# Performance work log

Hardware: AMD Instinct MI355X
Metric: run time of the kernel (lower is better)

Reference implementation:

```python
import jax, jax.numpy as jnp
import numpy as np

BS = 4096
D = 256
TAU = 0.5
EPS = 1e-08          # eps added to negative-sum denominator (module arg)
COS_EPS = 1e-08      # nn.CosineSimilarity norm clamp


def setup_inputs() -> dict:
    key = jax.random.key(0)
    k1, k2 = jax.random.split(key)
    zi = jax.random.normal(k1, (BS, D), dtype=jnp.float32)
    zj = jax.random.normal(k2, (BS, D), dtype=jnp.float32)
    return {"zi": zi, "zj": zj}


def reference(zi, zj):
    bs = zi.shape[0]
    n = 2 * bs
    z = jnp.concatenate([zi, zj], axis=0)                       # [2bs, D]
    # cosine similarity = normalized dot products (norms clamped like torch)
    norm = jnp.linalg.norm(z, axis=-1, keepdims=True)
    zn = z / jnp.maximum(norm, COS_EPS)
    sim = jnp.matmul(zn, zn.T) / TAU                            # [2bs, 2bs]
    e = jnp.exp(sim)
    # positive pairs: row i pairs with column (i+bs) mod 2bs
    rows = jnp.arange(n)
    pair = jnp.concatenate([jnp.arange(bs) + bs, jnp.arange(bs)])
    sim_pos = e[rows, pair]                                     # [2bs]
    # negatives: all entries in a row except the diagonal
    sim_neg_sum = e.sum(axis=-1) - jnp.diagonal(e)              # [2bs]
    loss = jnp.mean(-jnp.log(sim_pos / (sim_neg_sum + EPS)))
    return loss
```

## Files before the change

kernel.cpp:

```cpp
#include <hip/hip_runtime.h>
#include <hip/hip_bf16.h>


#define N_ROWS 8192
#define BSZ    4096
#define DIM    256
#define INV_TAU 2.0f
#define EPS_REF 1e-8f
#define COS_EPS 1e-8f
#define NG2     64
#define NTILES  (NG2 * (NG2 + 1) / 2)
#define LSTRIDE 260

typedef __attribute__((ext_vector_type(4))) float f32x4;
typedef __attribute__((ext_vector_type(8))) int   v8i;
typedef union { int4 x[2]; v8i v; } frag32;

__device__ __forceinline__ float red16(float x) {
    x += __int_as_float(__builtin_amdgcn_update_dpp(0, __float_as_int(x), 0x121, 0xf, 0xf, false));
    x += __int_as_float(__builtin_amdgcn_update_dpp(0, __float_as_int(x), 0x122, 0xf, 0xf, false));
    x += __int_as_float(__builtin_amdgcn_update_dpp(0, __float_as_int(x), 0x124, 0xf, 0xf, false));
    x += __int_as_float(__builtin_amdgcn_update_dpp(0, __float_as_int(x), 0x128, 0xf, 0xf, false));
    return x;
}

__global__ __launch_bounds__(256) void knorm(const float* __restrict__ zi,
                                             const float* __restrict__ zj,
                                             unsigned char* __restrict__ znsw,
                                             float* __restrict__ out) {
    __shared__ float lds[16 * LSTRIDE];
    __shared__ float nrm[16];
    const int rg = blockIdx.x;
    const int t  = threadIdx.x;
    const int w  = t >> 6;
    const int l  = t & 63;
    const int row0 = rg * 16;
    if (rg == 0 && t == 0) out[0] = 0.f;

    #pragma unroll
    for (int s = 0; s < 4; ++s) {
        const int row = s * 4 + w;
        const int r   = row0 + row;
        const float* src = (r < BSZ) ? zi + (size_t)r * DIM + l * 4
                                     : zj + (size_t)(r - BSZ) * DIM + l * 4;
        const float4 v = *(const float4*)src;
        *(float4*)&lds[row * LSTRIDE + l * 4] = v;
        float ss = v.x*v.x + v.y*v.y + v.z*v.z + v.w*v.w;
        #pragma unroll
        for (int off = 32; off >= 1; off >>= 1) ss += __shfl_xor(ss, off);
        if (l == 0) nrm[row] = 1.0f / fmaxf(sqrtf(ss), COS_EPS);
    }
    __syncthreads();

    const int pi = t >> 6, fl = t & 63;
    const int h = pi >> 1, p = pi & 1;
    const int r16 = fl & 15, q = fl >> 4;
    const int k0 = h * 128 + q * 32 + p * 16;
    const float inv = nrm[r16];
    float f[16];
    #pragma unroll
    for (int j = 0; j < 16; ++j) f[j] = lds[r16 * LSTRIDE + k0 + j] * inv;
    int wd[4];
    #pragma unroll
    for (int g = 0; g < 4; ++g) {
        int a = 0;
        a = __builtin_amdgcn_cvt_pk_fp8_f32(f[g*4+0], f[g*4+1], a, false);
        a = __builtin_amdgcn_cvt_pk_fp8_f32(f[g*4+2], f[g*4+3], a, true);
        wd[g] = a;
    }
    *(int4*)(znsw + (size_t)rg * 4096 + pi * 1024 + fl * 16) =
        make_int4(wd[0], wd[1], wd[2], wd[3]);
}

__global__ __launch_bounds__(256, 3) void kgemm(const unsigned char* __restrict__ znsw,
                                                float* __restrict__ P,
                                                float* __restrict__ selfdot,
                                                float* __restrict__ pairdot) {
    __shared__ __align__(16) unsigned char pan[32768];
    const int w = threadIdx.x >> 6;
    const int l = threadIdx.x & 63;

    const int t = blockIdx.x;
    int Gi = (int)((129.0f - sqrtf(16641.0f - 8.0f * (float)t)) * 0.5f);
    while ((Gi + 1) * (129 - (Gi + 1)) / 2 <= t) ++Gi;
    while (Gi * (129 - Gi) / 2 > t) --Gi;
    const int Gj = Gi + (t - Gi * (129 - Gi) / 2);

    const char* srcA = (const char*)znsw + (size_t)Gi * 32768;
    #pragma unroll
    for (int sub = 0; sub < 8; ++sub) {
        const int off = sub * 4096 + w * 1024;
        __builtin_amdgcn_global_load_lds(
            (const __attribute__((address_space(1))) void*)(srcA + off + l * 16),
            (__attribute__((address_space(3))) void*)(&pan[off]), 16, 0, 0);
    }

    const int rh = w >> 1, ch = w & 1;
    const char* bbase = (const char*)znsw + (size_t)Gj * 32768 + ch * 16384 + l * 16;

    frag32 B[4];
    #pragma unroll
    for (int nt = 0; nt < 4; ++nt) {
        B[nt].x[0] = *(const int4*)(bbase + nt * 4096);
        B[nt].x[1] = *(const int4*)(bbase + nt * 4096 + 1024);
    }

    f32x4 acc[4][4];
    #pragma unroll
    for (int mt = 0; mt < 4; ++mt)
        #pragma unroll
        for (int nt = 0; nt < 4; ++nt)
            acc[mt][nt] = (f32x4){0.f, 0.f, 0.f, 0.f};

    __syncthreads();

    #pragma unroll
    for (int h = 0; h < 2; ++h) {
        if (h == 1) {
            #pragma unroll
            for (int nt = 0; nt < 4; ++nt) {
                B[nt].x[0] = *(const int4*)(bbase + nt * 4096 + 2048);
                B[nt].x[1] = *(const int4*)(bbase + nt * 4096 + 3072);
            }
        }
        #pragma unroll
        for (int mt = 0; mt < 4; ++mt) {
            frag32 A;
            const char* ap = (const char*)&pan[(rh * 4 + mt) * 4096 + h * 2048] + l * 16;
            A.x[0] = *(const int4*)(ap);
            A.x[1] = *(const int4*)(ap + 1024);
            #pragma unroll
            for (int nt = 0; nt < 4; ++nt)
                acc[mt][nt] = __builtin_amdgcn_mfma_scale_f32_16x16x128_f8f6f4(
                    A.v, B[nt].v, acc[mt][nt],
                    0, 0,
                    0, 0x7f7f7f7f,
                    0, 0x7f7f7f7f);
        }
    }

    const int c = l & 15, q = l >> 4;
    const int rsel = c - 4 * q;
    const bool vld = (rsel >= 0) && (rsel < 4);

    if ((Gi == Gj || Gj == Gi + 32) && rh == ch) {
        float dv[4];
        #pragma unroll
        for (int mt = 0; mt < 4; ++mt) {
            float d = acc[mt][mt][0];
            #pragma unroll
            for (int r = 1; r < 4; ++r)
                if (rsel == r) d = acc[mt][mt][r];
            dv[mt] = d;
        }
        if (vld) {
            float* dst = (Gi == Gj) ? selfdot : pairdot;
            #pragma unroll
            for (int mt = 0; mt < 4; ++mt)
                dst[Gi * 128 + rh * 64 + mt * 16 + c] = dv[mt];
        }
    }

    #pragma unroll
    for (int mt = 0; mt < 4; ++mt)
        #pragma unroll
        for (int nt = 0; nt < 4; ++nt)
            #pragma unroll
            for (int r = 0; r < 4; ++r)
                acc[mt][nt][r] = __expf(acc[mt][nt][r] * INV_TAU);

    float rs[4][4];
    #pragma unroll
    for (int mt = 0; mt < 4; ++mt)
        #pragma unroll
        for (int r = 0; r < 4; ++r)
            rs[mt][r] = red16(acc[mt][0][r] + acc[mt][1][r] + acc[mt][2][r] + acc[mt][3][r]);
    if (c == 0) {
        #pragma unroll
        for (int mt = 0; mt < 4; ++mt) {
            const f32x4 o4 = (f32x4){rs[mt][0], rs[mt][1], rs[mt][2], rs[mt][3]};
            __builtin_nontemporal_store(o4,
                (f32x4*)&P[(size_t)(Gj * 2 + ch) * N_ROWS + Gi * 128 + rh * 64 + mt * 16 + q * 4]);
        }
    }

    if (Gi != Gj) {
        float cs[4];
        #pragma unroll
        for (int nt = 0; nt < 4; ++nt) {
            float s = 0.f;
            #pragma unroll
            for (int mt = 0; mt < 4; ++mt)
                #pragma unroll
                for (int r = 0; r < 4; ++r)
                    s += acc[mt][nt][r];
            s += __shfl_xor(s, 16);
            s += __shfl_xor(s, 32);
            cs[nt] = s;
        }
        if (q == 0) {
            #pragma unroll
            for (int nt = 0; nt < 4; ++nt)
                __builtin_nontemporal_store(cs[nt],
                    &P[(size_t)(Gi * 2 + rh) * N_ROWS + Gj * 128 + ch * 64 + nt * 16 + c]);
        }
    }
}

__global__ __launch_bounds__(256) void kfinal(const float* __restrict__ P,
                                              const float* __restrict__ selfdot,
                                              const float* __restrict__ pairdot,
                                              float* __restrict__ out) {
    const int l = threadIdx.x & 63;
    const int w = threadIdx.x >> 6;
    const int row = blockIdx.x * 64 + l;
    float s = 0.f;
    #pragma unroll
    for (int st = 0; st < 32; ++st)
        s += P[(size_t)(w * 32 + st) * N_ROWS + row];
    __shared__ float wsum[4][64];
    wsum[w][l] = s;
    __syncthreads();
    if (w == 0) {
        const float tot = wsum[0][l] + wsum[1][l] + wsum[2][l] + wsum[3][l];
        const float selfe = __expf(selfdot[row] * INV_TAU);
        const float pd    = pairdot[(row < BSZ) ? row : row - BSZ];
        float loss = logf(tot - selfe + EPS_REF) - pd * INV_TAU;
        #pragma unroll
        for (int off = 32; off >= 1; off >>= 1) loss += __shfl_xor(loss, off);
        if (l == 0) atomicAdd(out, loss * (1.0f / (float)N_ROWS));
    }
}

extern "C" void kernel_launch(void* const* d_in, const int* in_sizes, int n_in,
                              void* d_out, int out_size, void* d_ws, size_t ws_size,
                              hipStream_t stream) {
    const float* zi = (const float*)d_in[0];
    const float* zj = (const float*)d_in[1];
    float* out = (float*)d_out;

    char* ws = (char*)d_ws;
    unsigned char* znsw = (unsigned char*)ws;
    float* P       = (float*)(ws + 2 * 1024 * 1024);
    float* selfdot = (float*)(ws + 6 * 1024 * 1024);
    float* pairdot = (float*)(ws + 6 * 1024 * 1024 + 32 * 1024);

    knorm <<<N_ROWS / 16, 256, 0, stream>>>(zi, zj, znsw, out);
    kgemm <<<NTILES, 256, 0, stream>>>(znsw, P, selfdot, pairdot);
    kfinal<<<N_ROWS / 64, 256, 0, stream>>>(P, selfdot, pairdot, out);
}
```

Measured before the change: 82.96 us.

## Fuse final loss reduction into GEMM via atomics and last-block tail

Partial row sums of exp(sim) are no longer written to a large partial-sum matrix for a separate reduction kernel. Each tile now atomically adds them into a per-row accumulator. The last block to finish, found through an atomic completion counter, computes the log terms and writes the mean loss. This removes the third kernel launch and the partial-matrix traffic. In exchange it adds contention from many float atomics, a serialized single-block tail over 8192 rows, and non-deterministic summation order.

```diff
diff --git a/kernel.cpp b/kernel.cpp
--- a/kernel.cpp
+++ b/kernel.cpp
@@ -27,7 +27,8 @@
 __global__ __launch_bounds__(256) void knorm(const float* __restrict__ zi,
                                              const float* __restrict__ zj,
                                              unsigned char* __restrict__ znsw,
-                                             float* __restrict__ out) {
+                                             float* __restrict__ rowsum,
+                                             unsigned int* __restrict__ done) {
     __shared__ float lds[16 * LSTRIDE];
     __shared__ float nrm[16];
     const int rg = blockIdx.x;
@@ -35,7 +36,9 @@
     const int w  = t >> 6;
     const int l  = t & 63;
     const int row0 = rg * 16;
-    if (rg == 0 && t == 0) out[0] = 0.f;
+
+    if (t < 16) rowsum[rg * 16 + t] = 0.f;
+    if (rg == 0 && t == 16) *done = 0u;
 
     #pragma unroll
     for (int s = 0; s < 4; ++s) {
@@ -73,10 +76,14 @@
 }
 
 __global__ __launch_bounds__(256, 3) void kgemm(const unsigned char* __restrict__ znsw,
-                                                float* __restrict__ P,
+                                                float* __restrict__ rowsum,
                                                 float* __restrict__ selfdot,
-                                                float* __restrict__ pairdot) {
+                                                float* __restrict__ pairdot,
+                                                unsigned int* __restrict__ done,
+                                                float* __restrict__ out) {
     __shared__ __align__(16) unsigned char pan[32768];
+    __shared__ float tailred[4];
+    __shared__ int   islast;
     const int w = threadIdx.x >> 6;
     const int l = threadIdx.x & 63;
 
@@ -157,7 +164,8 @@
             float* dst = (Gi == Gj) ? selfdot : pairdot;
             #pragma unroll
             for (int mt = 0; mt < 4; ++mt)
-                dst[Gi * 128 + rh * 64 + mt * 16 + c] = dv[mt];
+                __hip_atomic_store(&dst[Gi * 128 + rh * 64 + mt * 16 + c], dv[mt],
+                                   __ATOMIC_RELAXED, __HIP_MEMORY_SCOPE_AGENT);
         }
     }
 
@@ -177,11 +185,10 @@
             rs[mt][r] = red16(acc[mt][0][r] + acc[mt][1][r] + acc[mt][2][r] + acc[mt][3][r]);
     if (c == 0) {
         #pragma unroll
-        for (int mt = 0; mt < 4; ++mt) {
-            const f32x4 o4 = (f32x4){rs[mt][0], rs[mt][1], rs[mt][2], rs[mt][3]};
-            __builtin_nontemporal_store(o4,
-                (f32x4*)&P[(size_t)(Gj * 2 + ch) * N_ROWS + Gi * 128 + rh * 64 + mt * 16 + q * 4]);
-        }
+        for (int mt = 0; mt < 4; ++mt)
+            #pragma unroll
+            for (int r = 0; r < 4; ++r)
+                atomicAdd(&rowsum[Gi * 128 + rh * 64 + mt * 16 + q * 4 + r], rs[mt][r]);
     }
 
     if (Gi != Gj) {
@@ -201,35 +208,36 @@
         if (q == 0) {
             #pragma unroll
             for (int nt = 0; nt < 4; ++nt)
-                __builtin_nontemporal_store(cs[nt],
-                    &P[(size_t)(Gi * 2 + rh) * N_ROWS + Gj * 128 + ch * 64 + nt * 16 + c]);
-        }
-    }
-}
-
-__global__ __launch_bounds__(256) void kfinal(const float* __restrict__ P,
-                                              const float* __restrict__ selfdot,
-                                              const float* __restrict__ pairdot,
-                                              float* __restrict__ out) {
-    const int l = threadIdx.x & 63;
-    const int w = threadIdx.x >> 6;
-    const int row = blockIdx.x * 64 + l;
-    float s = 0.f;
-    #pragma unroll
-    for (int st = 0; st < 32; ++st)
-        s += P[(size_t)(w * 32 + st) * N_ROWS + row];
-    __shared__ float wsum[4][64];
-    wsum[w][l] = s;
-    __syncthreads();
-    if (w == 0) {
-        const float tot = wsum[0][l] + wsum[1][l] + wsum[2][l] + wsum[3][l];
-        const float selfe = __expf(selfdot[row] * INV_TAU);
-        const float pd    = pairdot[(row < BSZ) ? row : row - BSZ];
-        float loss = logf(tot - selfe + EPS_REF) - pd * INV_TAU;
-        #pragma unroll
-        for (int off = 32; off >= 1; off >>= 1) loss += __shfl_xor(loss, off);
-        if (l == 0) atomicAdd(out, loss * (1.0f / (float)N_ROWS));
-    }
+                atomicAdd(&rowsum[Gj * 128 + ch * 64 + nt * 16 + c], cs[nt]);
+        }
+    }
+
+    __syncthreads();
+    if (threadIdx.x == 0) {
+        unsigned int old = __hip_atomic_fetch_add(done, 1u, __ATOMIC_ACQ_REL,
+                                                  __HIP_MEMORY_SCOPE_AGENT);
+        islast = (old == NTILES - 1);
+    }
+    __syncthreads();
+    if (!islast) return;
+
+    float part = 0.f;
+    for (int i = 0; i < N_ROWS / 256; ++i) {
+        const int row = i * 256 + threadIdx.x;
+        const float tot = __hip_atomic_load(&rowsum[row], __ATOMIC_RELAXED,
+                                            __HIP_MEMORY_SCOPE_AGENT);
+        const float sd  = __hip_atomic_load(&selfdot[row], __ATOMIC_RELAXED,
+                                            __HIP_MEMORY_SCOPE_AGENT);
+        const float pd  = __hip_atomic_load(&pairdot[(row < BSZ) ? row : row - BSZ],
+                                            __ATOMIC_RELAXED, __HIP_MEMORY_SCOPE_AGENT);
+        part += logf(tot - __expf(sd * INV_TAU) + EPS_REF) - pd * INV_TAU;
+    }
+    #pragma unroll
+    for (int off = 32; off >= 1; off >>= 1) part += __shfl_xor(part, off);
+    if (l == 0) tailred[w] = part;
+    __syncthreads();
+    if (threadIdx.x == 0)
+        out[0] = (tailred[0] + tailred[1] + tailred[2] + tailred[3]) * (1.0f / (float)N_ROWS);
 }
 
 extern "C" void kernel_launch(void* const* d_in, const int* in_sizes, int n_in,
@@ -241,11 +249,11 @@
 
     char* ws = (char*)d_ws;
     unsigned char* znsw = (unsigned char*)ws;
-    float* P       = (float*)(ws + 2 * 1024 * 1024);
-    float* selfdot = (float*)(ws + 6 * 1024 * 1024);
-    float* pairdot = (float*)(ws + 6 * 1024 * 1024 + 32 * 1024);
-
-    knorm <<<N_ROWS / 16, 256, 0, stream>>>(zi, zj, znsw, out);
-    kgemm <<<NTILES, 256, 0, stream>>>(znsw, P, selfdot, pairdot);
-    kfinal<<<N_ROWS / 64, 256, 0, stream>>>(P, selfdot, pairdot, out);
-}
+    float* rowsum  = (float*)(ws + 2 * 1024 * 1024);
+    float* selfdot = (float*)(ws + 2 * 1024 * 1024 + 32 * 1024);
+    float* pairdot = (float*)(ws + 2 * 1024 * 1024 + 64 * 1024);
+    unsigned int* done = (unsigned int*)(ws + 2 * 1024 * 1024 + 80 * 1024);
+
+    knorm <<<N_ROWS / 16, 256, 0, stream>>>(zi, zj, znsw, rowsum, done);
+    kgemm <<<NTILES, 256, 0, stream>>>(znsw, rowsum, selfdot, pairdot, done, out);
+}
```

New measurement: 116.7 us. +40.7%, slower.

## Fuse GEMM and final reduction into persistent kernel with grid-wide atomic barrier

Applied to the files above, without the earlier changes.

Merges the tile GEMM kernel and the final loss reduction into one persistent kernel of 512 blocks that loop over the triangular tiles. A global atomic counter acts as a grid barrier, after which the first 128 blocks run the per-row reduction and loss accumulation. This removes one kernel launch and the launch gap between them. In exchange, the former vector nontemporal stores become scalar relaxed atomic stores, and the spin-wait assumes all 512 blocks are co-resident, which risks deadlock if occupancy is lower.

```diff
diff --git a/kernel.cpp b/kernel.cpp
--- a/kernel.cpp
+++ b/kernel.cpp
@@ -10,6 +10,8 @@
 #define COS_EPS 1e-8f
 #define NG2     64
 #define NTILES  (NG2 * (NG2 + 1) / 2)
+#define GRID2   512
+#define PH3BLK  128
 #define LSTRIDE 260
 
 typedef __attribute__((ext_vector_type(4))) float f32x4;
@@ -27,6 +29,7 @@
 __global__ __launch_bounds__(256) void knorm(const float* __restrict__ zi,
                                              const float* __restrict__ zj,
                                              unsigned char* __restrict__ znsw,
+                                             unsigned int* __restrict__ cnt,
                                              float* __restrict__ out) {
     __shared__ float lds[16 * LSTRIDE];
     __shared__ float nrm[16];
@@ -35,7 +38,8 @@
     const int w  = t >> 6;
     const int l  = t & 63;
     const int row0 = rg * 16;
-    if (rg == 0 && t == 0) out[0] = 0.f;
+    if (rg == 0 && t == 0)  out[0] = 0.f;
+    if (rg == 0 && t == 16) *cnt = 0u;
 
     #pragma unroll
     for (int s = 0; s < 4; ++s) {
@@ -72,159 +76,173 @@
         make_int4(wd[0], wd[1], wd[2], wd[3]);
 }
 
-__global__ __launch_bounds__(256, 3) void kgemm(const unsigned char* __restrict__ znsw,
-                                                float* __restrict__ P,
-                                                float* __restrict__ selfdot,
-                                                float* __restrict__ pairdot) {
+__global__ __launch_bounds__(256, 3) void kfused(const unsigned char* __restrict__ znsw,
+                                                 float* __restrict__ P,
+                                                 float* __restrict__ selfdot,
+                                                 float* __restrict__ pairdot,
+                                                 unsigned int* __restrict__ cnt,
+                                                 float* __restrict__ out) {
     __shared__ __align__(16) unsigned char pan[32768];
+    __shared__ float wsum[4][64];
     const int w = threadIdx.x >> 6;
     const int l = threadIdx.x & 63;
-
-    const int t = blockIdx.x;
-    int Gi = (int)((129.0f - sqrtf(16641.0f - 8.0f * (float)t)) * 0.5f);
-    while ((Gi + 1) * (129 - (Gi + 1)) / 2 <= t) ++Gi;
-    while (Gi * (129 - Gi) / 2 > t) --Gi;
-    const int Gj = Gi + (t - Gi * (129 - Gi) / 2);
-
-    const char* srcA = (const char*)znsw + (size_t)Gi * 32768;
-    #pragma unroll
-    for (int sub = 0; sub < 8; ++sub) {
-        const int off = sub * 4096 + w * 1024;
-        __builtin_amdgcn_global_load_lds(
-            (const __attribute__((address_space(1))) void*)(srcA + off + l * 16),
-            (__attribute__((address_space(3))) void*)(&pan[off]), 16, 0, 0);
-    }
-
     const int rh = w >> 1, ch = w & 1;
-    const char* bbase = (const char*)znsw + (size_t)Gj * 32768 + ch * 16384 + l * 16;
-
-    frag32 B[4];
-    #pragma unroll
-    for (int nt = 0; nt < 4; ++nt) {
-        B[nt].x[0] = *(const int4*)(bbase + nt * 4096);
-        B[nt].x[1] = *(const int4*)(bbase + nt * 4096 + 1024);
-    }
-
-    f32x4 acc[4][4];
-    #pragma unroll
-    for (int mt = 0; mt < 4; ++mt)
-        #pragma unroll
-        for (int nt = 0; nt < 4; ++nt)
-            acc[mt][nt] = (f32x4){0.f, 0.f, 0.f, 0.f};
-
-    __syncthreads();
-
-    #pragma unroll
-    for (int h = 0; h < 2; ++h) {
-        if (h == 1) {
-            #pragma unroll
-            for (int nt = 0; nt < 4; ++nt) {
-                B[nt].x[0] = *(const int4*)(bbase + nt * 4096 + 2048);
-                B[nt].x[1] = *(const int4*)(bbase + nt * 4096 + 3072);
-            }
-        }
-        #pragma unroll
-        for (int mt = 0; mt < 4; ++mt) {
-            frag32 A;
-            const char* ap = (const char*)&pan[(rh * 4 + mt) * 4096 + h * 2048] + l * 16;
-            A.x[0] = *(const int4*)(ap);
-            A.x[1] = *(const int4*)(ap + 1024);
-            #pragma unroll
-            for (int nt = 0; nt < 4; ++nt)
-                acc[mt][nt] = __builtin_amdgcn_mfma_scale_f32_16x16x128_f8f6f4(
-                    A.v, B[nt].v, acc[mt][nt],
-                    0, 0,
-                    0, 0x7f7f7f7f,
-                    0, 0x7f7f7f7f);
-        }
-    }
-
     const int c = l & 15, q = l >> 4;
     const int rsel = c - 4 * q;
     const bool vld = (rsel >= 0) && (rsel < 4);
 
-    if ((Gi == Gj || Gj == Gi + 32) && rh == ch) {
-        float dv[4];
-        #pragma unroll
-        for (int mt = 0; mt < 4; ++mt) {
-            float d = acc[mt][mt][0];
-            #pragma unroll
-            for (int r = 1; r < 4; ++r)
-                if (rsel == r) d = acc[mt][mt][r];
-            dv[mt] = d;
-        }
-        if (vld) {
-            float* dst = (Gi == Gj) ? selfdot : pairdot;
+    for (int t = blockIdx.x; t < NTILES; t += GRID2) {
+        int Gi = (int)((129.0f - sqrtf(16641.0f - 8.0f * (float)t)) * 0.5f);
+        while ((Gi + 1) * (129 - (Gi + 1)) / 2 <= t) ++Gi;
+        while (Gi * (129 - Gi) / 2 > t) --Gi;
+        const int Gj = Gi + (t - Gi * (129 - Gi) / 2);
+
+        __syncthreads();
+
+        const char* srcA = (const char*)znsw + (size_t)Gi * 32768;
+        #pragma unroll
+        for (int sub = 0; sub < 8; ++sub) {
+            const int off = sub * 4096 + w * 1024;
+            __builtin_amdgcn_global_load_lds(
+                (const __attribute__((address_space(1))) void*)(srcA + off + l * 16),
+                (__attribute__((address_space(3))) void*)(&pan[off]), 16, 0, 0);
+        }
+
+        const char* bbase = (const char*)znsw + (size_t)Gj * 32768 + ch * 16384 + l * 16;
+
+        frag32 B[4];
+        #pragma unroll
+        for (int nt = 0; nt < 4; ++nt) {
+            B[nt].x[0] = *(const int4*)(bbase + nt * 4096);
+            B[nt].x[1] = *(const int4*)(bbase + nt * 4096 + 1024);
+        }
+
+        f32x4 acc[4][4];
+        #pragma unroll
+        for (int mt = 0; mt < 4; ++mt)
+            #pragma unroll
+            for (int nt = 0; nt < 4; ++nt)
+                acc[mt][nt] = (f32x4){0.f, 0.f, 0.f, 0.f};
+
+        __syncthreads();
+
+        #pragma unroll
+        for (int h = 0; h < 2; ++h) {
+            if (h == 1) {
+                #pragma unroll
+                for (int nt = 0; nt < 4; ++nt) {
+                    B[nt].x[0] = *(const int4*)(bbase + nt * 4096 + 2048);
+                    B[nt].x[1] = *(const int4*)(bbase + nt * 4096 + 3072);
+                }
+            }
+            #pragma unroll
+            for (int mt = 0; mt < 4; ++mt) {
+                frag32 A;
+                const char* ap = (const char*)&pan[(rh * 4 + mt) * 4096 + h * 2048] + l * 16;
+                A.x[0] = *(const int4*)(ap);
+                A.x[1] = *(const int4*)(ap + 1024);
+                #pragma unroll
+                for (int nt = 0; nt < 4; ++nt)
+                    acc[mt][nt] = __builtin_amdgcn_mfma_scale_f32_16x16x128_f8f6f4(
+                        A.v, B[nt].v, acc[mt][nt],
+                        0, 0,
+                        0, 0x7f7f7f7f,
+                        0, 0x7f7f7f7f);
+            }
+        }
+
+        if ((Gi == Gj || Gj == Gi + 32) && rh == ch) {
+            float dv[4];
+            #pragma unroll
+            for (int mt = 0; mt < 4; ++mt) {
+                float d = acc[mt][mt][0];
+                #pragma unroll
+                for (int r = 1; r < 4; ++r)
+                    if (rsel == r) d = acc[mt][mt][r];
+                dv[mt] = d;
+            }
+            if (vld) {
+                float* dst = (Gi == Gj) ? selfdot : pairdot;
+                #pragma unroll
+                for (int mt = 0; mt < 4; ++mt)
+                    __hip_atomic_store(&dst[Gi * 128 + rh * 64 + mt * 16 + c], dv[mt],
+                                       __ATOMIC_RELAXED, __HIP_MEMORY_SCOPE_AGENT);
+            }
+        }
+
+        #pragma unroll
+        for (int mt = 0; mt < 4; ++mt)
+            #pragma unroll
+            for (int nt = 0; nt < 4; ++nt)
+                #pragma unroll
+                for (int r = 0; r < 4; ++r)
+                    acc[mt][nt][r] = __expf(acc[mt][nt][r] * INV_TAU);
+
+        float rs[4][4];
+        #pragma unroll
+        for (int mt = 0; mt < 4; ++mt)
+            #pragma unroll
+            for (int r = 0; r < 4; ++r)
+                rs[mt][r] = red16(acc[mt][0][r] + acc[mt][1][r] + acc[mt][2][r] + acc[mt][3][r]);
+        if (c == 0) {
             #pragma unroll
             for (int mt = 0; mt < 4; ++mt)
-                dst[Gi * 128 + rh * 64 + mt * 16 + c] = dv[mt];
-        }
-    }
-
-    #pragma unroll
-    for (int mt = 0; mt < 4; ++mt)
-        #pragma unroll
-        for (int nt = 0; nt < 4; ++nt)
-            #pragma unroll
-            for (int r = 0; r < 4; ++r)
-                acc[mt][nt][r] = __expf(acc[mt][nt][r] * INV_TAU);
-
-    float rs[4][4];
-    #pragma unroll
-    for (int mt = 0; mt < 4; ++mt)
-        #pragma unroll
-        for (int r = 0; r < 4; ++r)
-            rs[mt][r] = red16(acc[mt][0][r] + acc[mt][1][r] + acc[mt][2][r] + acc[mt][3][r]);
-    if (c == 0) {
-        #pragma unroll
-        for (int mt = 0; mt < 4; ++mt) {
-            const f32x4 o4 = (f32x4){rs[mt][0], rs[mt][1], rs[mt][2], rs[mt][3]};
-            __builtin_nontemporal_store(o4,
-                (f32x4*)&P[(size_t)(Gj * 2 + ch) * N_ROWS + Gi * 128 + rh * 64 + mt * 16 + q * 4]);
-        }
-    }
-
-    if (Gi != Gj) {
-        float cs[4];
-        #pragma unroll
-        for (int nt = 0; nt < 4; ++nt) {
-            float s = 0.f;
-            #pragma unroll
-            for (int mt = 0; mt < 4; ++mt)
                 #pragma unroll
                 for (int r = 0; r < 4; ++r)
-                    s += acc[mt][nt][r];
-            s += __shfl_xor(s, 16);
-            s += __shfl_xor(s, 32);
-            cs[nt] = s;
-        }
-        if (q == 0) {
-            #pragma unroll
-            for (int nt = 0; nt < 4; ++nt)
-                __builtin_nontemporal_store(cs[nt],
-                    &P[(size_t)(Gi * 2 + rh) * N_ROWS + Gj * 128 + ch * 64 + nt * 16 + c]);
-        }
-    }
-}
-
-__global__ __launch_bounds__(256) void kfinal(const float* __restrict__ P,
-                                              const float* __restrict__ selfdot,
-                                              const float* __restrict__ pairdot,
-                                              float* __restrict__ out) {
-    const int l = threadIdx.x & 63;
-    const int w = threadIdx.x >> 6;
+                    __hip_atomic_store(
+                        &P[(size_t)(Gj * 2 + ch) * N_ROWS + Gi * 128 + rh * 64 + mt * 16 + q * 4 + r],
+                        rs[mt][r], __ATOMIC_RELAXED, __HIP_MEMORY_SCOPE_AGENT);
+        }
+
+        if (Gi != Gj) {
+            float cs[4];
+            #pragma unroll
+            for (int nt = 0; nt < 4; ++nt) {
+                float s = 0.f;
+                #pragma unroll
+                for (int mt = 0; mt < 4; ++mt)
+                    #pragma unroll
+                    for (int r = 0; r < 4; ++r)
+                        s += acc[mt][nt][r];
+                s += __shfl_xor(s, 16);
+                s += __shfl_xor(s, 32);
+                cs[nt] = s;
+            }
+            if (q == 0) {
+                #pragma unroll
+                for (int nt = 0; nt < 4; ++nt)
+                    __hip_atomic_store(
+                        &P[(size_t)(Gi * 2 + rh) * N_ROWS + Gj * 128 + ch * 64 + nt * 16 + c],
+                        cs[nt], __ATOMIC_RELAXED, __HIP_MEMORY_SCOPE_AGENT);
+            }
+        }
+    }
+
+    __syncthreads();
+    if (threadIdx.x == 0)
+        __hip_atomic_fetch_add(cnt, 1u, __ATOMIC_ACQ_REL, __HIP_MEMORY_SCOPE_AGENT);
+    if (blockIdx.x >= PH3BLK) return;
+
+    if (threadIdx.x == 0) {
+        while (__hip_atomic_load(cnt, __ATOMIC_ACQUIRE, __HIP_MEMORY_SCOPE_AGENT) < GRID2)
+            __builtin_amdgcn_s_sleep(8);
+    }
+    __syncthreads();
+
     const int row = blockIdx.x * 64 + l;
     float s = 0.f;
     #pragma unroll
     for (int st = 0; st < 32; ++st)
-        s += P[(size_t)(w * 32 + st) * N_ROWS + row];
-    __shared__ float wsum[4][64];
+        s += __hip_atomic_load(&P[(size_t)(w * 32 + st) * N_ROWS + row],
+                               __ATOMIC_RELAXED, __HIP_MEMORY_SCOPE_AGENT);
     wsum[w][l] = s;
     __syncthreads();
     if (w == 0) {
         const float tot = wsum[0][l] + wsum[1][l] + wsum[2][l] + wsum[3][l];
-        const float selfe = __expf(selfdot[row] * INV_TAU);
-        const float pd    = pairdot[(row < BSZ) ? row : row - BSZ];
+        const float selfe = __expf(__hip_atomic_load(&selfdot[row], __ATOMIC_RELAXED,
+                                                     __HIP_MEMORY_SCOPE_AGENT) * INV_TAU);
+        const float pd = __hip_atomic_load(&pairdot[(row < BSZ) ? row : row - BSZ],
+                                           __ATOMIC_RELAXED, __HIP_MEMORY_SCOPE_AGENT);
         float loss = logf(tot - selfe + EPS_REF) - pd * INV_TAU;
         #pragma unroll
         for (int off = 32; off >= 1; off >>= 1) loss += __shfl_xor(loss, off);
@@ -244,8 +262,8 @@
     float* P       = (float*)(ws + 2 * 1024 * 1024);
     float* selfdot = (float*)(ws + 6 * 1024 * 1024);
     float* pairdot = (float*)(ws + 6 * 1024 * 1024 + 32 * 1024);
-
-    knorm <<<N_ROWS / 16, 256, 0, stream>>>(zi, zj, znsw, out);
-    kgemm <<<NTILES, 256, 0, stream>>>(znsw, P, selfdot, pairdot);
-    kfinal<<<N_ROWS / 64, 256, 0, stream>>>(P, selfdot, pairdot, out);
-}
+    unsigned int* cnt = (unsigned int*)(ws + 6 * 1024 * 1024 + 48 * 1024);
+
+    knorm <<<N_ROWS / 16, 256, 0, stream>>>(zi, zj, znsw, cnt, out);
+    kfused<<<GRID2, 256, 0, stream>>>(znsw, P, selfdot, pairdot, cnt, out);
+}
```

Result: slower. 128.5 us (+54.9%).

## Fuse final reduction into GEMM kernel via grid-wide atomic completion counter

Applied to the files above, without the earlier changes.

Removes the separate kfinal launch by having the last 128 GEMM blocks spin-wait on a set of striped atomic counters until all tiles have finished, then perform the per-row reduction and loss accumulation. The counters are reset in knorm. The P stores switch from nontemporal to normal stores, so the later in-kernel reads are more likely to hit in cache. This saves one kernel launch and its gap, at the cost of spin-waiting blocks occupying CUs, and it relies on every earlier block being scheduled before the waiting blocks.

```diff
diff --git a/kernel.cpp b/kernel.cpp
--- a/kernel.cpp
+++ b/kernel.cpp
@@ -10,6 +10,8 @@
 #define COS_EPS 1e-8f
 #define NG2     64
 #define NTILES  (NG2 * (NG2 + 1) / 2)
+#define PH3BLK  128
+#define NCNT    32
 #define LSTRIDE 260
 
 typedef __attribute__((ext_vector_type(4))) float f32x4;
@@ -27,6 +29,7 @@
 __global__ __launch_bounds__(256) void knorm(const float* __restrict__ zi,
                                              const float* __restrict__ zj,
                                              unsigned char* __restrict__ znsw,
+                                             unsigned int* __restrict__ cnt,
                                              float* __restrict__ out) {
     __shared__ float lds[16 * LSTRIDE];
     __shared__ float nrm[16];
@@ -36,6 +39,7 @@
     const int l  = t & 63;
     const int row0 = rg * 16;
     if (rg == 0 && t == 0) out[0] = 0.f;
+    if (rg == 0 && t < NCNT) cnt[t * 16] = 0u;
 
     #pragma unroll
     for (int s = 0; s < 4; ++s) {
@@ -72,11 +76,14 @@
         make_int4(wd[0], wd[1], wd[2], wd[3]);
 }
 
-__global__ __launch_bounds__(256, 3) void kgemm(const unsigned char* __restrict__ znsw,
-                                                float* __restrict__ P,
-                                                float* __restrict__ selfdot,
-                                                float* __restrict__ pairdot) {
+__global__ __launch_bounds__(256, 3) void kfused(const unsigned char* __restrict__ znsw,
+                                                 float* __restrict__ P,
+                                                 float* __restrict__ selfdot,
+                                                 float* __restrict__ pairdot,
+                                                 unsigned int* __restrict__ cnt,
+                                                 float* __restrict__ out) {
     __shared__ __align__(16) unsigned char pan[32768];
+    __shared__ float wsum[4][64];
     const int w = threadIdx.x >> 6;
     const int l = threadIdx.x & 63;
 
@@ -177,11 +184,9 @@
             rs[mt][r] = red16(acc[mt][0][r] + acc[mt][1][r] + acc[mt][2][r] + acc[mt][3][r]);
     if (c == 0) {
         #pragma unroll
-        for (int mt = 0; mt < 4; ++mt) {
-            const f32x4 o4 = (f32x4){rs[mt][0], rs[mt][1], rs[mt][2], rs[mt][3]};
-            __builtin_nontemporal_store(o4,
-                (f32x4*)&P[(size_t)(Gj * 2 + ch) * N_ROWS + Gi * 128 + rh * 64 + mt * 16 + q * 4]);
-        }
+        for (int mt = 0; mt < 4; ++mt)
+            *(f32x4*)&P[(size_t)(Gj * 2 + ch) * N_ROWS + Gi * 128 + rh * 64 + mt * 16 + q * 4] =
+                (f32x4){rs[mt][0], rs[mt][1], rs[mt][2], rs[mt][3]};
     }
 
     if (Gi != Gj) {
@@ -201,24 +206,35 @@
         if (q == 0) {
             #pragma unroll
             for (int nt = 0; nt < 4; ++nt)
-                __builtin_nontemporal_store(cs[nt],
-                    &P[(size_t)(Gi * 2 + rh) * N_ROWS + Gj * 128 + ch * 64 + nt * 16 + c]);
-        }
-    }
-}
-
-__global__ __launch_bounds__(256) void kfinal(const float* __restrict__ P,
-                                              const float* __restrict__ selfdot,
-                                              const float* __restrict__ pairdot,
-                                              float* __restrict__ out) {
-    const int l = threadIdx.x & 63;
-    const int w = threadIdx.x >> 6;
-    const int row = blockIdx.x * 64 + l;
+                P[(size_t)(Gi * 2 + rh) * N_ROWS + Gj * 128 + ch * 64 + nt * 16 + c] = cs[nt];
+        }
+    }
+
+    __syncthreads();
+    if (threadIdx.x == 0)
+        __hip_atomic_fetch_add(&cnt[(blockIdx.x & (NCNT - 1)) * 16], 1u,
+                               __ATOMIC_ACQ_REL, __HIP_MEMORY_SCOPE_AGENT);
+    if (blockIdx.x < NTILES - PH3BLK) return;
+
+    if (threadIdx.x == 0) {
+        unsigned int total;
+        do {
+            total = 0;
+            #pragma unroll
+            for (int i = 0; i < NCNT; ++i)
+                total += __hip_atomic_load(&cnt[i * 16], __ATOMIC_ACQUIRE,
+                                           __HIP_MEMORY_SCOPE_AGENT);
+            if (total < NTILES) __builtin_amdgcn_s_sleep(1);
+        } while (total < NTILES);
+    }
+    __syncthreads();
+
+    const int fb  = blockIdx.x - (NTILES - PH3BLK);
+    const int row = fb * 64 + l;
     float s = 0.f;
     #pragma unroll
     for (int st = 0; st < 32; ++st)
         s += P[(size_t)(w * 32 + st) * N_ROWS + row];
-    __shared__ float wsum[4][64];
     wsum[w][l] = s;
     __syncthreads();
     if (w == 0) {
@@ -244,8 +260,8 @@
     float* P       = (float*)(ws + 2 * 1024 * 1024);
     float* selfdot = (float*)(ws + 6 * 1024 * 1024);
     float* pairdot = (float*)(ws + 6 * 1024 * 1024 + 32 * 1024);
-
-    knorm <<<N_ROWS / 16, 256, 0, stream>>>(zi, zj, znsw, out);
-    kgemm <<<NTILES, 256, 0, stream>>>(znsw, P, selfdot, pairdot);
-    kfinal<<<N_ROWS / 64, 256, 0, stream>>>(P, selfdot, pairdot, out);
-}
+    unsigned int* cnt = (unsigned int*)(ws + 6 * 1024 * 1024 + 48 * 1024);
+
+    knorm <<<N_ROWS / 16, 256, 0, stream>>>(zi, zj, znsw, cnt, out);
+    kfused<<<NTILES, 256, 0, stream>>>(znsw, P, selfdot, pairdot, cnt, out);
+}
```

Measured after the change: 182.7 us. +120.2%, slower.
